# Kernel tuning notes

Measured on AMD Instinct MI355X. Metric: run time of the kernel, lower is better.

Reference implementation:

```python
import jax, jax.numpy as jnp
import numpy as np

B, S, D, H = 2, 2048, 1024, 16
HD = D // H  # head dim = 64


def setup_inputs() -> dict:
    key = jax.random.key(0)
    k1, k2, k3, k4 = jax.random.split(key, 4)
    x = jax.random.normal(k1, (B, S, D), dtype=jnp.float32)
    context = jax.random.normal(k2, (B, S, D), dtype=jnp.float32)
    Wq = jax.random.normal(k3, (D, D), dtype=jnp.float32) * 0.02   # to_query weight [out,in]
    Wkv = jax.random.normal(k4, (2 * D, D), dtype=jnp.float32) * 0.02  # to_key_value weight [out,in]
    return {"x": x, "context": context, "Wq": Wq, "Wkv": Wkv}


def reference(x, context, Wq, Wkv):
    b, i, _ = x.shape
    j = context.shape[1]
    # projections (torch Linear: y = x @ W.T)
    q = x @ Wq.T                      # [b, i, D]
    kv = context @ Wkv.T              # [b, j, 2D]
    k, v = kv[..., :D], kv[..., D:]
    # split heads: (h c) ordering -> reshape last dim to [H, HD]
    q = q.reshape(b, i, H, HD).transpose(0, 2, 1, 3)  # [b,h,i,c]
    k = k.reshape(b, j, H, HD).transpose(0, 2, 1, 3)  # [b,h,j,c]
    v = v.reshape(b, j, H, HD).transpose(0, 2, 1, 3)  # [b,h,j,c]
    q = q * (HD ** -0.5)
    scores = jnp.einsum('bhic,bhjc->bhij', q, k)      # [b,h,i,j]
    scores = scores - jax.lax.stop_gradient(scores.max(axis=-1, keepdims=True))
    attn = jax.nn.softmax(scores, axis=-1)
    out = jnp.einsum('bhij,bhjc->bhic', attn, v)      # [b,h,i,c]
    out = out.transpose(0, 2, 1, 3).reshape(b, i, H * HD)  # 'b h n d -> b n (h d)'
    return out
```

## Files before the change

### kernel.cpp

```cpp
#include <hip/hip_runtime.h>
#include <hip/hip_bf16.h>
#include <stdint.h>

typedef unsigned short u16;
typedef __attribute__((ext_vector_type(8))) __bf16 bf16x8;
typedef __attribute__((ext_vector_type(4))) float f32x4;
typedef __attribute__((ext_vector_type(16))) float f32x16;

#define AS1(p) ((const __attribute__((address_space(1))) void*)(p))
#define AS3(p) ((__attribute__((address_space(3))) void*)(p))

__device__ __forceinline__ u16 f2bf(float f) {
  union { float f; uint32_t u; } c; c.f = f;
  uint32_t u = c.u;
  u += 0x7fffu + ((u >> 16) & 1u);
  return (u16)(u >> 16);
}

__device__ __forceinline__ float exp2_fast(float x) {
  float r; asm("v_exp_f32 %0, %1" : "=v"(r) : "v"(x)); return r;
}

__global__ __launch_bounds__(256) void cast4_f32_bf16(
    const float4* __restrict__ s0, ushort4* __restrict__ d0, int n0,
    const float4* __restrict__ s1, ushort4* __restrict__ d1, int n1,
    const float4* __restrict__ s2, ushort4* __restrict__ d2, int n2,
    const float4* __restrict__ s3, ushort4* __restrict__ d3, int n3) {
  int bid = blockIdx.x;
  const float4* src; ushort4* dst; int n4, b0, nb;
  if (bid < 512)       { src = s0; dst = d0; n4 = n0; b0 = 0;    nb = 512; }
  else if (bid < 1024) { src = s1; dst = d1; n4 = n1; b0 = 512;  nb = 512; }
  else if (bid < 1152) { src = s2; dst = d2; n4 = n2; b0 = 1024; nb = 128; }
  else                 { src = s3; dst = d3; n4 = n3; b0 = 1152; nb = 256; }
  int stride = nb * 256;
  for (int i = (bid - b0) * 256 + threadIdx.x; i < n4; i += stride) {
    float4 v = src[i];
    ushort4 o;
    o.x = f2bf(v.x); o.y = f2bf(v.y); o.z = f2bf(v.z); o.w = f2bf(v.w);
    dst[i] = o;
  }
}

__global__ __launch_bounds__(256) void gemm_fused(const u16* __restrict__ xb,
                                                  const u16* __restrict__ wqb,
                                                  u16* __restrict__ qo,
                                                  const u16* __restrict__ cb,
                                                  const u16* __restrict__ wkb,
                                                  u16* __restrict__ kvo,
                                                  float scale_q) {
  __shared__ u16 As[3][128 * 32];
  __shared__ u16 Bs[3][128 * 32];
  const int K = 1024;
  int bid = (blockIdx.x & 7) * 96 + (blockIdx.x >> 3);
  const u16 *A, *B; u16* C; int N, bm, bn; float scale;
  if (bid < 256) { A = xb; B = wqb; C = qo;  N = 1024; bm = bid >> 3; bn = bid & 7;  scale = scale_q; }
  else { int b2 = bid - 256; A = cb; B = wkb; C = kvo; N = 2048; bm = b2 >> 4; bn = b2 & 15; scale = 1.0f; }

  int tid = threadIdx.x;
  int w = tid >> 6, l = tid & 63;
  int wr = w >> 1, wc = w & 1;
  int lr = l & 15, lg = l >> 4;

  const u16* Abase = A + (size_t)(bm * 128 + (l >> 2)) * K + (l & 3) * 8;
  const u16* Bbase = B + (size_t)(bn * 128 + (l >> 2)) * K + (l & 3) * 8;

  f32x4 acc[4][4];
#pragma unroll
  for (int i = 0; i < 4; ++i)
#pragma unroll
    for (int j = 0; j < 4; ++j) acc[i][j] = (f32x4){0.f, 0.f, 0.f, 0.f};

#define STAGE(buf, k0)                                                              \
  {                                                                                 \
    _Pragma("unroll")                                                               \
    for (int t2 = 0; t2 < 2; ++t2) {                                                \
      int seg = w * 2 + t2;                                                         \
      __builtin_amdgcn_global_load_lds(AS1(Abase + (size_t)seg * 16 * K + (k0)),    \
                                       AS3(&As[buf][seg * 512]), 16, 0, 0);         \
      __builtin_amdgcn_global_load_lds(AS1(Bbase + (size_t)seg * 16 * K + (k0)),    \
                                       AS3(&Bs[buf][seg * 512]), 16, 0, 0);         \
    }                                                                               \
  }

  STAGE(0, 0);
  STAGE(1, 32);
  int cur = 0;
  for (int t = 0; t < 32; ++t) {
    if (t < 30) {
      int pf = cur + 2; if (pf >= 3) pf -= 3;
      STAGE(pf, (t + 2) * 32);
      asm volatile("s_waitcnt vmcnt(8)" ::: "memory");
    } else if (t == 30) {
      asm volatile("s_waitcnt vmcnt(4)" ::: "memory");
    } else {
      asm volatile("s_waitcnt vmcnt(0)" ::: "memory");
    }
    __builtin_amdgcn_s_barrier();
    bf16x8 af[4], bb[4];
#pragma unroll
    for (int i = 0; i < 4; ++i)
      af[i] = *(const bf16x8*)(&As[cur][(wr * 64 + i * 16 + lr) * 32 + lg * 8]);
#pragma unroll
    for (int j = 0; j < 4; ++j)
      bb[j] = *(const bf16x8*)(&Bs[cur][(wc * 64 + j * 16 + lr) * 32 + lg * 8]);
    asm volatile("s_waitcnt lgkmcnt(0)" ::: "memory");
    __builtin_amdgcn_sched_barrier(0);
#pragma unroll
    for (int i = 0; i < 4; ++i)
#pragma unroll
      for (int j = 0; j < 4; ++j)
        acc[i][j] = __builtin_amdgcn_mfma_f32_16x16x32_bf16(af[i], bb[j], acc[i][j], 0, 0, 0);
    __builtin_amdgcn_s_barrier();
    if (++cur == 3) cur = 0;
  }
#undef STAGE

#pragma unroll
  for (int i = 0; i < 4; ++i)
#pragma unroll
    for (int j = 0; j < 4; ++j)
#pragma unroll
      for (int r = 0; r < 4; ++r) {
        int row = bm * 128 + wr * 64 + i * 16 + lg * 4 + r;
        int col = bn * 128 + wc * 64 + j * 16 + lr;
        C[(size_t)row * N + col] = f2bf(acc[i][j][r] * scale);
      }
}

#define SQ 2048
#define NTT 16

__global__ __launch_bounds__(256, 2) void attn_kernel(const u16* __restrict__ Q,
                                                      const u16* __restrict__ KV,
                                                      float* __restrict__ O) {
  __shared__ u16 Ks[2][128 * 64];
  __shared__ u16 Vt[2][64 * 128];

  int wgid = (blockIdx.x & 7) * 64 + (blockIdx.x >> 3);
  int qt = wgid & 15;
  int bh = wgid >> 4;
  int b = bh >> 4, h = bh & 15;
  int tid = threadIdx.x;
  int w = tid >> 6, l = tid & 63;
  int li = l & 31, hi = l >> 5;
  int jr = l >> 3, bk = l & 7;
  int a7 = tid & 7, jj = tid >> 3;

  const u16* kbase = KV + (size_t)b * SQ * 2048 + (size_t)h * 64;
  const u16* vbase = kbase + 1024;
  int i0g = qt * 128 + w * 32;
  const u16* qrow = Q + (size_t)(b * SQ + i0g + li) * 1024 + h * 64;

  bf16x8 qf0 = *(const bf16x8*)(qrow + 0  + hi * 8);
  bf16x8 qf1 = *(const bf16x8*)(qrow + 16 + hi * 8);
  bf16x8 qf2 = *(const bf16x8*)(qrow + 32 + hi * 8);
  bf16x8 qf3 = *(const bf16x8*)(qrow + 48 + hi * 8);

#pragma unroll
  for (int c = 0; c < 4; ++c) {
    const u16* gk = kbase + (size_t)(c * 32 + w * 8 + jr) * 2048 + ((bk ^ jr) * 8);
    __builtin_amdgcn_global_load_lds(AS1(gk), AS3(&Ks[0][c * 2048 + w * 512]), 16, 0, 0);
  }
  uint4 vrA = *(const uint4*)(vbase + (size_t)(jj +  0) * 2048 + a7 * 8);
  uint4 vrB = *(const uint4*)(vbase + (size_t)(jj + 32) * 2048 + a7 * 8);
  uint4 vrC = *(const uint4*)(vbase + (size_t)(jj + 64) * 2048 + a7 * 8);
  uint4 vrD = *(const uint4*)(vbase + (size_t)(jj + 96) * 2048 + a7 * 8);

  float m_run = -1e30f, l_run = 0.f;
  f32x16 acc0, acc1, zz;
#pragma unroll
  for (int r = 0; r < 16; ++r) { acc0[r] = 0.f; acc1[r] = 0.f; zz[r] = 0.f; }

  int swk = (li & 7) << 4;
  int sw0 = ((li ^ (li >> 3)) & 7) << 4;
  int sw1 = (((32 + li) ^ ((32 + li) >> 3)) & 7) << 4;

  for (int t = 0; t < NTT; ++t) {
    u16* Ksc = (u16*)Ks[t & 1];
    char* Vtc = (char*)Vt[t & 1];
    __syncthreads();
    {
      const u16* pA = (const u16*)&vrA;
      const u16* pB = (const u16*)&vrB;
      const u16* pC = (const u16*)&vrC;
      const u16* pD = (const u16*)&vrD;
#pragma unroll
      for (int e = 0; e < 8; ++e) {
        int dbyte = (a7 * 8 + e) * 256, sw = (e ^ a7) << 4;
        *(u16*)(Vtc + dbyte + (((jj * 2) +   0) ^ sw)) = pA[e];
        *(u16*)(Vtc + dbyte + (((jj * 2) +  64) ^ sw)) = pB[e];
        *(u16*)(Vtc + dbyte + (((jj * 2) + 128) ^ sw)) = pC[e];
        *(u16*)(Vtc + dbyte + (((jj * 2) + 192) ^ sw)) = pD[e];
      }
    }
    asm volatile("s_waitcnt lgkmcnt(0)" ::: "memory");
    __builtin_amdgcn_s_barrier();
    if (t + 1 < NTT) {
      int j0n = (t + 1) * 128;
      u16* Ksn = (u16*)Ks[(t + 1) & 1];
#pragma unroll
      for (int c = 0; c < 4; ++c) {
        const u16* gk = kbase + (size_t)(j0n + c * 32 + w * 8 + jr) * 2048 + ((bk ^ jr) * 8);
        __builtin_amdgcn_global_load_lds(AS1(gk), AS3(&Ksn[c * 2048 + w * 512]), 16, 0, 0);
      }
      vrA = *(const uint4*)(vbase + (size_t)(j0n + jj +  0) * 2048 + a7 * 8);
      vrB = *(const uint4*)(vbase + (size_t)(j0n + jj + 32) * 2048 + a7 * 8);
      vrC = *(const uint4*)(vbase + (size_t)(j0n + jj + 64) * 2048 + a7 * 8);
      vrD = *(const uint4*)(vbase + (size_t)(j0n + jj + 96) * 2048 + a7 * 8);
    }
    f32x16 s0, s1, s2, s3;
    __builtin_amdgcn_s_setprio(1);
#define QKT1(sv, JB)                                                             \
    {                                                                            \
      const char* kr = (const char*)Ksc + ((JB) * 32 + li) * 128;                \
      bf16x8 kk;                                                                 \
      kk = *(const bf16x8*)(kr + ((0  + hi * 16) ^ swk));                        \
      sv = __builtin_amdgcn_mfma_f32_32x32x16_bf16(kk, qf0, zz, 0, 0, 0);        \
      kk = *(const bf16x8*)(kr + ((32 + hi * 16) ^ swk));                        \
      sv = __builtin_amdgcn_mfma_f32_32x32x16_bf16(kk, qf1, sv, 0, 0, 0);        \
      kk = *(const bf16x8*)(kr + ((64 + hi * 16) ^ swk));                        \
      sv = __builtin_amdgcn_mfma_f32_32x32x16_bf16(kk, qf2, sv, 0, 0, 0);        \
      kk = *(const bf16x8*)(kr + ((96 + hi * 16) ^ swk));                        \
      sv = __builtin_amdgcn_mfma_f32_32x32x16_bf16(kk, qf3, sv, 0, 0, 0);        \
    }
    QKT1(s0, 0)
    QKT1(s1, 1)
    QKT1(s2, 2)
    QKT1(s3, 3)
#undef QKT1
    __builtin_amdgcn_s_setprio(0);
    float pm = fmaxf(s0[14], s0[15]);
#pragma unroll
    for (int r = 0; r < 14; r += 2) pm = fmaxf(fmaxf(pm, s0[r]), s0[r + 1]);
#pragma unroll
    for (int r = 0; r < 16; r += 2) pm = fmaxf(fmaxf(pm, s1[r]), s1[r + 1]);
#pragma unroll
    for (int r = 0; r < 16; r += 2) pm = fmaxf(fmaxf(pm, s2[r]), s2[r + 1]);
#pragma unroll
    for (int r = 0; r < 16; r += 2) pm = fmaxf(fmaxf(pm, s3[r]), s3[r + 1]);
    pm = fmaxf(pm, __shfl_xor(pm, 32));
    if (!__all(pm <= m_run + 8.0f)) {
      float mnew = fmaxf(m_run, pm);
      float esc = exp2_fast(m_run - mnew);
      m_run = mnew;
      l_run *= esc;
#pragma unroll
      for (int r = 0; r < 16; ++r) { acc0[r] *= esc; acc1[r] *= esc; }
    }
    float sum = 0.f;
#pragma unroll
    for (int r = 0; r < 16; ++r) { s0[r] = exp2_fast(s0[r] - m_run); sum += s0[r]; }
#pragma unroll
    for (int r = 0; r < 16; ++r) { s1[r] = exp2_fast(s1[r] - m_run); sum += s1[r]; }
#pragma unroll
    for (int r = 0; r < 16; ++r) { s2[r] = exp2_fast(s2[r] - m_run); sum += s2[r]; }
#pragma unroll
    for (int r = 0; r < 16; ++r) { s3[r] = exp2_fast(s3[r] - m_run); sum += s3[r]; }
    sum += __shfl_xor(sum, 32);
    l_run += sum;
    unsigned pw[32];
#pragma unroll
    for (int i2 = 0; i2 < 8; ++i2) {
      asm("v_cvt_pk_bf16_f32 %0, %1, %2" : "=v"(pw[i2])      : "v"(s0[2 * i2]), "v"(s0[2 * i2 + 1]));
      asm("v_cvt_pk_bf16_f32 %0, %1, %2" : "=v"(pw[8 + i2])  : "v"(s1[2 * i2]), "v"(s1[2 * i2 + 1]));
      asm("v_cvt_pk_bf16_f32 %0, %1, %2" : "=v"(pw[16 + i2]) : "v"(s2[2 * i2]), "v"(s2[2 * i2 + 1]));
      asm("v_cvt_pk_bf16_f32 %0, %1, %2" : "=v"(pw[24 + i2]) : "v"(s3[2 * i2]), "v"(s3[2 * i2 + 1]));
    }
#pragma unroll
    for (int gB = 0; gB < 4; ++gB) {
      int o = gB * 8;
      asm volatile("v_permlane32_swap_b32 %0, %1" : "+v"(pw[o + 0]), "+v"(pw[o + 2]));
      asm volatile("v_permlane32_swap_b32 %0, %1" : "+v"(pw[o + 1]), "+v"(pw[o + 3]));
      asm volatile("v_permlane32_swap_b32 %0, %1" : "+v"(pw[o + 4]), "+v"(pw[o + 6]));
      asm volatile("v_permlane32_swap_b32 %0, %1" : "+v"(pw[o + 5]), "+v"(pw[o + 7]));
    }
    __builtin_amdgcn_s_setprio(1);
#pragma unroll
    for (int jsp = 0; jsp < 8; ++jsp) {
      uint4 ufr;
      ufr.x = pw[jsp * 4 + 0]; ufr.y = pw[jsp * 4 + 1];
      ufr.z = pw[jsp * 4 + 2]; ufr.w = pw[jsp * 4 + 3];
      bf16x8 pa = *(bf16x8*)&ufr;
      int jbyte = jsp * 32 + hi * 16;
      bf16x8 v0 = *(const bf16x8*)(Vtc + li * 256 + (jbyte ^ sw0));
      bf16x8 v1 = *(const bf16x8*)(Vtc + (32 + li) * 256 + (jbyte ^ sw1));
      acc0 = __builtin_amdgcn_mfma_f32_32x32x16_bf16(v0, pa, acc0, 0, 0, 0);
      acc1 = __builtin_amdgcn_mfma_f32_32x32x16_bf16(v1, pa, acc1, 0, 0, 0);
    }
    __builtin_amdgcn_s_setprio(0);
  }
  float inv = 1.f / l_run;
  float* orow = O + ((size_t)(b * SQ + i0g + li) * 1024 + h * 64);
#pragma unroll
  for (int g = 0; g < 4; ++g) {
    f32x4 o0, o1;
#pragma unroll
    for (int q_ = 0; q_ < 4; ++q_) {
      o0[q_] = acc0[g * 4 + q_] * inv;
      o1[q_] = acc1[g * 4 + q_] * inv;
    }
    *(f32x4*)(orow + 8 * g + 4 * hi) = o0;
    *(f32x4*)(orow + 32 + 8 * g + 4 * hi) = o1;
  }
}

extern "C" void kernel_launch(void* const* d_in, const int* in_sizes, int n_in,
                              void* d_out, int out_size, void* d_ws, size_t ws_size,
                              hipStream_t stream) {
  (void)in_sizes; (void)n_in; (void)out_size; (void)ws_size;
  const float* x   = (const float*)d_in[0];
  const float* ctx = (const float*)d_in[1];
  const float* Wq  = (const float*)d_in[2];
  const float* Wkv = (const float*)d_in[3];
  float* out = (float*)d_out;
  char* ws = (char*)d_ws;

  u16* xb  = (u16*)(ws);
  u16* cb  = (u16*)(ws + (8ull  << 20));
  u16* wqb = (u16*)(ws + (16ull << 20));
  u16* wkb = (u16*)(ws + (18ull << 20));
  u16* q   = (u16*)(ws + (22ull << 20));
  u16* kv  = (u16*)(ws + (30ull << 20));

  cast4_f32_bf16<<<1408, 256, 0, stream>>>(
      (const float4*)x,   (ushort4*)xb,  (4096 * 1024) / 4,
      (const float4*)ctx, (ushort4*)cb,  (4096 * 1024) / 4,
      (const float4*)Wq,  (ushort4*)wqb, (1024 * 1024) / 4,
      (const float4*)Wkv, (ushort4*)wkb, (2048 * 1024) / 4);

  gemm_fused<<<768, 256, 0, stream>>>(xb, wqb, q, cb, wkb, kv, 0.125f * 1.44269504f);

  attn_kernel<<<512, 256, 0, stream>>>(q, kv, out);
}
```

Baseline: 99.01 us.

## Single-buffer V tile, raise occupancy, compute softmax row sums with MFMA

Drops the double buffer for the transposed V tile in LDS and raises the launch bound from 2 to 3 blocks per CU, so more workgroups can be resident. The per-row softmax denominator is no longer summed with scalar adds and a cross-lane shuffle. Instead an extra MFMA multiplies a ones matrix by the probability fragment into a separate accumulator. This adds a third MFMA per PV step and 16 more accumulator registers, which could cause spills under the tighter register budget. It also loses the overlap the second V buffer gave between staging the next tile and reading the current one.

```diff
diff --git a/kernel.cpp b/kernel.cpp
--- a/kernel.cpp
+++ b/kernel.cpp
@@ -130,11 +130,11 @@
 #define SQ 2048
 #define NTT 16
 
-__global__ __launch_bounds__(256, 2) void attn_kernel(const u16* __restrict__ Q,
+__global__ __launch_bounds__(256, 3) void attn_kernel(const u16* __restrict__ Q,
                                                       const u16* __restrict__ KV,
                                                       float* __restrict__ O) {
   __shared__ u16 Ks[2][128 * 64];
-  __shared__ u16 Vt[2][64 * 128];
+  __shared__ u16 Vt[64 * 128];
 
   int wgid = (blockIdx.x & 7) * 64 + (blockIdx.x >> 3);
   int qt = wgid & 15;
@@ -156,6 +156,11 @@
   bf16x8 qf2 = *(const bf16x8*)(qrow + 32 + hi * 8);
   bf16x8 qf3 = *(const bf16x8*)(qrow + 48 + hi * 8);
 
+  union { u16 u[8]; bf16x8 v; } onesu;
+#pragma unroll
+  for (int e = 0; e < 8; ++e) onesu.u[e] = 0x3F80;
+  bf16x8 ones = onesu.v;
+
 #pragma unroll
   for (int c = 0; c < 4; ++c) {
     const u16* gk = kbase + (size_t)(c * 32 + w * 8 + jr) * 2048 + ((bk ^ jr) * 8);
@@ -166,10 +171,10 @@
   uint4 vrC = *(const uint4*)(vbase + (size_t)(jj + 64) * 2048 + a7 * 8);
   uint4 vrD = *(const uint4*)(vbase + (size_t)(jj + 96) * 2048 + a7 * 8);
 
-  float m_run = -1e30f, l_run = 0.f;
-  f32x16 acc0, acc1, zz;
-#pragma unroll
-  for (int r = 0; r < 16; ++r) { acc0[r] = 0.f; acc1[r] = 0.f; zz[r] = 0.f; }
+  float m_run = -1e30f;
+  f32x16 acc0, acc1, accS, zz;
+#pragma unroll
+  for (int r = 0; r < 16; ++r) { acc0[r] = 0.f; acc1[r] = 0.f; accS[r] = 0.f; zz[r] = 0.f; }
 
   int swk = (li & 7) << 4;
   int sw0 = ((li ^ (li >> 3)) & 7) << 4;
@@ -177,7 +182,7 @@
 
   for (int t = 0; t < NTT; ++t) {
     u16* Ksc = (u16*)Ks[t & 1];
-    char* Vtc = (char*)Vt[t & 1];
+    char* Vtc = (char*)Vt;
     __syncthreads();
     {
       const u16* pA = (const u16*)&vrA;
@@ -243,21 +248,18 @@
       float mnew = fmaxf(m_run, pm);
       float esc = exp2_fast(m_run - mnew);
       m_run = mnew;
-      l_run *= esc;
+      accS[0] *= esc;
 #pragma unroll
       for (int r = 0; r < 16; ++r) { acc0[r] *= esc; acc1[r] *= esc; }
     }
-    float sum = 0.f;
-#pragma unroll
-    for (int r = 0; r < 16; ++r) { s0[r] = exp2_fast(s0[r] - m_run); sum += s0[r]; }
-#pragma unroll
-    for (int r = 0; r < 16; ++r) { s1[r] = exp2_fast(s1[r] - m_run); sum += s1[r]; }
-#pragma unroll
-    for (int r = 0; r < 16; ++r) { s2[r] = exp2_fast(s2[r] - m_run); sum += s2[r]; }
-#pragma unroll
-    for (int r = 0; r < 16; ++r) { s3[r] = exp2_fast(s3[r] - m_run); sum += s3[r]; }
-    sum += __shfl_xor(sum, 32);
-    l_run += sum;
+#pragma unroll
+    for (int r = 0; r < 16; ++r) s0[r] = exp2_fast(s0[r] - m_run);
+#pragma unroll
+    for (int r = 0; r < 16; ++r) s1[r] = exp2_fast(s1[r] - m_run);
+#pragma unroll
+    for (int r = 0; r < 16; ++r) s2[r] = exp2_fast(s2[r] - m_run);
+#pragma unroll
+    for (int r = 0; r < 16; ++r) s3[r] = exp2_fast(s3[r] - m_run);
     unsigned pw[32];
 #pragma unroll
     for (int i2 = 0; i2 < 8; ++i2) {
@@ -286,10 +288,11 @@
       bf16x8 v1 = *(const bf16x8*)(Vtc + (32 + li) * 256 + (jbyte ^ sw1));
       acc0 = __builtin_amdgcn_mfma_f32_32x32x16_bf16(v0, pa, acc0, 0, 0, 0);
       acc1 = __builtin_amdgcn_mfma_f32_32x32x16_bf16(v1, pa, acc1, 0, 0, 0);
+      accS = __builtin_amdgcn_mfma_f32_32x32x16_bf16(ones, pa, accS, 0, 0, 0);
     }
     __builtin_amdgcn_s_setprio(0);
   }
-  float inv = 1.f / l_run;
+  float inv = 1.f / accS[0];
   float* orow = O + ((size_t)(b * SQ + i0g + li) * 1024 + h * 64);
 #pragma unroll
   for (int g = 0; g < 4; ++g) {
```

Measured after the change: 330.1 us. 3.33x slower.
